# Performance work log

Measured on AMD Instinct MI355X. Metric: run time of the kernel, lower is better.

Reference implementation:

```python
import jax, jax.numpy as jnp
import numpy as np

GRID_H, GRID_W = 128, 128
MODES1, MODES2 = 24, 24
DEPTH = 4
WIDTH = 64
IN_CH = 3
OUT_CH = 1
B, N = 8, 16384
EPS = 1e-5


def _gelu(x):
    return jax.nn.gelu(x, approximate=False)  # torch default (erf) GELU


def setup_inputs() -> dict:
    key = jax.random.key(0)
    ks = jax.random.split(key, 16)
    f32 = jnp.float32

    def lin(k, i, o, std=None):
        s = std if std is not None else 1.0 / np.sqrt(i)
        return (jax.random.normal(k, (i, o), f32) * s).astype(f32)

    scale = 1.0 / (WIDTH * WIDTH)
    sw_shape = (DEPTH, WIDTH, WIDTH, MODES1, MODES2)
    return {
        'coords': jax.random.uniform(ks[0], (B, N, 2), f32, -1.0, 1.0),
        'features': jax.random.normal(ks[1], (B, N, IN_CH), f32),
        'dw0': lin(ks[2], 2, 32), 'db0': jnp.zeros((32,), f32),
        'dw1': lin(ks[3], 32, 32), 'db1': jnp.zeros((32,), f32),
        'dw2': lin(ks[4], 32, 2, std=0.01), 'db2': jnp.zeros((2,), f32),
        'lift_w': lin(ks[5], IN_CH + 2, WIDTH), 'lift_b': jnp.zeros((WIDTH,), f32),
        'sw1r': scale * jax.random.uniform(ks[6], sw_shape, f32),
        'sw1i': scale * jax.random.uniform(ks[7], sw_shape, f32),
        'sw2r': scale * jax.random.uniform(ks[8], sw_shape, f32),
        'sw2i': scale * jax.random.uniform(ks[9], sw_shape, f32),
        'pw_w': (jax.random.normal(ks[10], (DEPTH, WIDTH, WIDTH), f32) / np.sqrt(WIDTH)).astype(f32),
        'pw_b': jnp.zeros((DEPTH, WIDTH), f32),
        'p1_w': lin(ks[11], WIDTH, 128), 'p1_b': jnp.zeros((128,), f32),
        'p2_w': lin(ks[12], 128, OUT_CH), 'p2_b': jnp.zeros((OUT_CH,), f32),
    }


def _spectral_conv2d(x, w1, w2):
    # x: (B, C, H, W); w1/w2: (C_in, C_out, MODES1, MODES2) complex
    Bb, C, H, W = x.shape
    x_ft = jnp.fft.rfft2(x)  # (B, C, H, W//2+1)
    lo = jnp.einsum('bixy,ioxy->boxy', x_ft[:, :, :MODES1, :MODES2], w1)
    hi = jnp.einsum('bixy,ioxy->boxy', x_ft[:, :, -MODES1:, :MODES2], w2)
    out_ft = jnp.zeros((Bb, WIDTH, H, W // 2 + 1), jnp.complex64)
    out_ft = out_ft.at[:, :, :MODES1, :MODES2].set(lo)
    out_ft = out_ft.at[:, :, -MODES1:, :MODES2].set(hi)
    return jnp.fft.irfft2(out_ft, s=(H, W))


def _forward(coords, features, dw0, db0, dw1, db1, dw2, db2, lift_w, lift_b,
             sw1r, sw1i, sw2r, sw2i, pw_w, pw_b, p1_w, p1_b, p2_w, p2_b):
    Bb, Nn, _ = coords.shape
    # 1) deformation: latent = x + MLP(x), clamped to [-1, 1]
    h = _gelu(coords @ dw0 + db0)
    h = _gelu(h @ dw1 + db1)
    latent = jnp.clip(coords + (h @ dw2 + db2), -1.0, 1.0)
    # 2) lifting on concat(features, coords)
    feat = jnp.concatenate([features, coords], axis=-1) @ lift_w + lift_b  # (B,N,width)
    # 3) P2G: nearest-neighbor scatter-mean onto latent grid (align_corners=True)
    ph = (latent[..., 0] + 1.0) * 0.5 * (GRID_H - 1)
    pw = (latent[..., 1] + 1.0) * 0.5 * (GRID_W - 1)
    ih = jnp.clip(jnp.round(ph).astype(jnp.int32), 0, GRID_H - 1)
    iw = jnp.clip(jnp.round(pw).astype(jnp.int32), 0, GRID_W - 1)
    boff = jnp.arange(Bb, dtype=jnp.int32)[:, None] * (GRID_H * GRID_W)
    flat = (boff + ih * GRID_W + iw).reshape(-1)
    nseg = Bb * GRID_H * GRID_W
    sums = jax.ops.segment_sum(feat.reshape(-1, WIDTH), flat, num_segments=nseg)
    cnts = jax.ops.segment_sum(jnp.ones((Bb * Nn, 1), feat.dtype), flat, num_segments=nseg)
    grid = (sums / jnp.maximum(cnts, 1.0)).reshape(Bb, GRID_H, GRID_W, WIDTH)
    grid = grid.transpose(0, 3, 1, 2)  # (B, width, H, W)
    # 4) FNO blocks: gelu(instnorm(spectral(x) + pointwise(x)))
    for d in range(DEPTH):
        w1 = sw1r[d] + 1j * sw1i[d]
        w2 = sw2r[d] + 1j * sw2i[d]
        y = _spectral_conv2d(grid, w1, w2)
        y = y + jnp.einsum('bihw,io->bohw', grid, pw_w[d]) + pw_b[d][None, :, None, None]
        mu = y.mean(axis=(2, 3), keepdims=True)
        var = y.var(axis=(2, 3), keepdims=True)
        grid = _gelu((y - mu) * jax.lax.rsqrt(var + EPS))
    # 5) G2P: bilinear sample latent grid at latent coords
    h0 = jnp.floor(ph)
    w0 = jnp.floor(pw)
    th = (ph - h0)[:, None, :]
    tw = (pw - w0)[:, None, :]
    h0i = jnp.clip(h0.astype(jnp.int32), 0, GRID_H - 1)
    h1i = jnp.clip(h0i + 1, 0, GRID_H - 1)
    w0i = jnp.clip(w0.astype(jnp.int32), 0, GRID_W - 1)
    w1i = jnp.clip(w0i + 1, 0, GRID_W - 1)
    gridf = grid.reshape(Bb, WIDTH, GRID_H * GRID_W)

    def gather(hi_, wi_):
        idx = (hi_ * GRID_W + wi_)[:, None, :]  # (B,1,N)
        return jnp.take_along_axis(gridf, idx, axis=2)  # (B,width,N)

    v00 = gather(h0i, w0i)
    v01 = gather(h0i, w1i)
    v10 = gather(h1i, w0i)
    v11 = gather(h1i, w1i)
    sampled = (v00 * (1 - th) * (1 - tw) + v01 * (1 - th) * tw
               + v10 * th * (1 - tw) + v11 * th * tw)
    sampled = sampled.transpose(0, 2, 1)  # (B,N,width)
    # 6) projection (dropout is identity at eval)
    out = _gelu(sampled @ p1_w + p1_b) @ p2_w + p2_b
    return out  # (B, N, out_channels)


def reference(coords, features, dw0, db0, dw1, db1, dw2, db2, lift_w, lift_b,
              sw1r, sw1i, sw2r, sw2i, pw_w, pw_b, p1_w, p1_b, p2_w, p2_b):
    return _forward(coords, features, dw0, db0, dw1, db1, dw2, db2, lift_w, lift_b,
                    sw1r, sw1i, sw2r, sw2i, pw_w, pw_b, p1_w, p1_b, p2_w, p2_b)
```

## Files before the change

### kernel.cpp

```cpp
#include <hip/hip_runtime.h>
#include <math.h>

#define GH 128
#define GW 128
#define HWC 16384
#define NMODE 1152
#define PI_F 3.14159265358979323846f

typedef _Float16 f16;
typedef __attribute__((ext_vector_type(8))) _Float16 f16x8;
typedef __attribute__((ext_vector_type(4))) float f32x4;

__device__ __forceinline__ float gelu_f(float x) {
  return 0.5f * x * (1.0f + erff(x * 0.70710678118654752f));
}

__device__ __forceinline__ float gelu_fast(float x) {
  float ax = fabsf(x) * 0.70710678118654752f;
  float t = 1.f / fmaf(0.3275911f, ax, 1.f);
  float p = t * fmaf(t, fmaf(t, fmaf(t, fmaf(t, 1.061405429f, -1.453152027f),
                                     1.421413741f), -0.284496736f), 0.254829592f);
  float e = __expf(-ax * ax);
  float r = 1.f - p * e;
  r = copysignf(r, x);
  return 0.5f * x * (1.f + r);
}

__global__ __launch_bounds__(256) void k_twiddle(f16* __restrict__ Fw, f16* __restrict__ Fh,
                                                 f16* __restrict__ Bh, f16* __restrict__ Bw,
                                                 const float* __restrict__ p1w, f16* __restrict__ p1t)
{
  int idx = blockIdx.x * 256 + threadIdx.x;
  if (idx < 6144) {
    int n = idx >> 7, w = idx & 127;
    int ky = n >> 1;
    int ang = (ky * w) & 127;
    float s, c; sincosf((float)ang * (PI_F / 64.f), &s, &c);
    Fw[idx] = (f16)((n & 1) ? -s : c);
  } else if (idx < 18432) {
    int t = idx - 6144;
    int n = t >> 7, h = t & 127;
    int kx = n < 48 ? n : n - 48;
    int f = kx < 24 ? kx : kx + 80;
    int ang = (f * h) & 127;
    float s, c; sincosf((float)ang * (PI_F / 64.f), &s, &c);
    float v = (n < 48) ? c : s;
    Fh[t] = (f16)v;
    Bh[h * 96 + n] = (f16)v;
  } else if (idx < 26624) {
    int t = idx - 18432;
    int w = t >> 6, k = t & 63;
    float v = 0.f;
    if (k < 48 && k != 1) {
      int ky = k >> 1;
      float g = (ky == 0) ? 1.f : 2.f;
      int ang = (ky * w) & 127;
      float s, c; sincosf((float)ang * (PI_F / 64.f), &s, &c);
      v = (k & 1) ? -g * s : g * c;
    }
    Bw[t] = (f16)v;
  } else if (idx < 34816) {
    int t = idx - 26624;
    int j = t >> 6, i = t & 63;
    p1t[t] = (f16)p1w[i * 128 + j];
  }
}

__global__ __launch_bounds__(256) void k_points(
    const float* __restrict__ coords,
    const float* __restrict__ dw0, const float* __restrict__ db0,
    const float* __restrict__ dw1, const float* __restrict__ db1,
    const float* __restrict__ dw2, const float* __restrict__ db2,
    int* __restrict__ cnt_i,
    int* __restrict__ ptrank, int* __restrict__ pd_cell,
    int* __restrict__ pd_idx, float* __restrict__ pd_th, float* __restrict__ pd_tw)
{
  int pid = blockIdx.x * 256 + threadIdx.x;
  float2 c = ((const float2*)coords)[pid];

  float h1[32];
#pragma unroll
  for (int j = 0; j < 32; ++j)
    h1[j] = gelu_f(fmaf(c.x, dw0[j], fmaf(c.y, dw0[32 + j], db0[j])));

  float a[32];
#pragma unroll
  for (int j = 0; j < 32; ++j) a[j] = db1[j];
#pragma unroll 4
  for (int k = 0; k < 32; ++k) {
    float hk = h1[k];
    const float* wr = dw1 + k * 32;
#pragma unroll
    for (int j = 0; j < 32; ++j) a[j] = fmaf(hk, wr[j], a[j]);
  }

  float d0 = db2[0], d1 = db2[1];
#pragma unroll 4
  for (int k = 0; k < 32; ++k) {
    float hk = gelu_f(a[k]);
    d0 = fmaf(hk, dw2[2 * k], d0);
    d1 = fmaf(hk, dw2[2 * k + 1], d1);
  }

  float l0 = fminf(fmaxf(c.x + d0, -1.f), 1.f);
  float l1 = fminf(fmaxf(c.y + d1, -1.f), 1.f);
  float ph = (l0 + 1.f) * 0.5f * 127.f;
  float pw = (l1 + 1.f) * 0.5f * 127.f;
  int ih = min(max((int)rintf(ph), 0), 127);
  int iw = min(max((int)rintf(pw), 0), 127);
  int b = pid >> 14;
  int cell = b * HWC + ih * GW + iw;

  int r = atomicAdd(&cnt_i[cell], 1);
  ptrank[pid] = r;
  pd_cell[pid] = cell;

  float fh = floorf(ph), fw = floorf(pw);
  int h0i = min(max((int)fh, 0), 127), w0i = min(max((int)fw, 0), 127);
  pd_idx[pid] = h0i | (w0i << 8);
  pd_th[pid] = ph - fh;
  pd_tw[pid] = pw - fw;
}

__global__ __launch_bounds__(256) void k_scanA(const int* __restrict__ cnt,
                                               int* __restrict__ starts, int* __restrict__ btot)
{
  __shared__ int sh[256];
  int blk = blockIdx.x, t = threadIdx.x;
  int base = blk * 512;
  int v0 = cnt[base + 2 * t], v1 = cnt[base + 2 * t + 1];
  int pair = v0 + v1;
  sh[t] = pair; __syncthreads();
  int acc = pair;
  for (int off = 1; off < 256; off <<= 1) {
    int add = (t >= off) ? sh[t - off] : 0;
    __syncthreads();
    acc += add; sh[t] = acc;
    __syncthreads();
  }
  int excl = acc - pair;
  starts[base + 2 * t] = excl;
  starts[base + 2 * t + 1] = excl + v0;
  if (t == 255) btot[blk] = acc;
}

__global__ __launch_bounds__(256) void k_scanB(const int* __restrict__ btot, int* __restrict__ boff)
{
  __shared__ int sh[256];
  int t = threadIdx.x;
  int v = btot[t];
  sh[t] = v; __syncthreads();
  int acc = v;
  for (int off = 1; off < 256; off <<= 1) {
    int add = (t >= off) ? sh[t - off] : 0;
    __syncthreads();
    acc += add; sh[t] = acc;
    __syncthreads();
  }
  boff[t] = acc - v;
}

__global__ __launch_bounds__(256) void k_perm(const int* __restrict__ pd_cell, const int* __restrict__ ptrank,
                                              const int* __restrict__ starts, const int* __restrict__ boff,
                                              const int* __restrict__ pd_idx, const float* __restrict__ pd_th,
                                              const float* __restrict__ pd_tw,
                                              const float* __restrict__ coords, const float* __restrict__ feats,
                                              int4* __restrict__ pds,
                                              float4* __restrict__ scA, float* __restrict__ scB)
{
  int pid = blockIdx.x * 256 + threadIdx.x;
  int cell = pd_cell[pid];
  int dst = starts[cell] + boff[cell >> 9] + ptrank[pid];
  int4 rec;
  rec.x = pid;
  rec.y = pd_idx[pid];
  rec.z = __float_as_int(pd_th[pid]);
  rec.w = __float_as_int(pd_tw[pid]);
  pds[dst] = rec;
  float2 c = ((const float2*)coords)[pid];
  scA[dst] = make_float4(feats[pid * 3], feats[pid * 3 + 1], feats[pid * 3 + 2], c.x);
  scB[dst] = c.y;
}

__global__ __launch_bounds__(256) void k_gridlift(const float4* __restrict__ scA, const float* __restrict__ scB,
                                                  const int* __restrict__ starts, const int* __restrict__ boff,
                                                  const int* __restrict__ cnt_i,
                                                  const float* __restrict__ lw,
                                                  const float* __restrict__ lb,
                                                  f16* __restrict__ Gh)
{
  __shared__ float sp[2][128][5];
  __shared__ float s_lw[5][64];
  __shared__ float s_lb[64];
  __shared__ float s_cnt[128];
  int b = blockIdx.y, cbase = blockIdx.x * 128, tid = threadIdx.x;
  int cl = tid & 127, par = tid >> 7;
  int gcell = b * HWC + cbase + cl;
  int start = starts[gcell] + boff[gcell >> 9];
  int cnt = cnt_i[gcell];
  float a0 = 0.f, a1 = 0.f, a2 = 0.f, a3 = 0.f, a4 = 0.f;
  for (int p = start + par; p < start + cnt; p += 2) {
    float4 A = scA[p];
    a0 += A.x; a1 += A.y; a2 += A.z; a3 += A.w; a4 += scB[p];
  }
  sp[par][cl][0] = a0; sp[par][cl][1] = a1; sp[par][cl][2] = a2;
  sp[par][cl][3] = a3; sp[par][cl][4] = a4;
  if (par == 0) s_cnt[cl] = (float)cnt;
  for (int l = tid; l < 320; l += 256) ((float*)s_lw)[l] = lw[l];
  if (tid < 64) s_lb[tid] = lb[tid];
  __syncthreads();
  float v0 = sp[0][cl][0] + sp[1][cl][0];
  float v1 = sp[0][cl][1] + sp[1][cl][1];
  float v2 = sp[0][cl][2] + sp[1][cl][2];
  float v3 = sp[0][cl][3] + sp[1][cl][3];
  float v4 = sp[0][cl][4] + sp[1][cl][4];
  float cntf = s_cnt[cl];
  float inv = 1.f / fmaxf(cntf, 1.f);
  int oh = tid >> 7;
#pragma unroll
  for (int j = 0; j < 32; ++j) {
    int o = oh * 32 + j;
    float val = cntf * s_lb[o];
    val = fmaf(v0, s_lw[0][o], val);
    val = fmaf(v1, s_lw[1][o], val);
    val = fmaf(v2, s_lw[2][o], val);
    val = fmaf(v3, s_lw[3][o], val);
    val = fmaf(v4, s_lw[4][o], val);
    Gh[(size_t)(b * 64 + o) * HWC + cbase + cl] = (f16)(val * inv);
  }
}

__global__ __launch_bounds__(256) void k_fwdpw(const f16* __restrict__ Gh,
                                               const f16* __restrict__ Fw_t, const f16* __restrict__ Fh_t,
                                               float2* __restrict__ Xf2,
                                               const float* __restrict__ pww, const float* __restrict__ pwb,
                                               f16* __restrict__ yh)
{
  __shared__ char smem[52224];
  int tid = threadIdx.x;
  int wave = tid >> 6, lane = tid & 63, lr = lane & 15, lg = lane >> 4;

  if (blockIdx.x < 512) {
    f16 (*s_fw)[136]  = (f16(*)[136])smem;
    f16 (*s_img)[136] = (f16(*)[136])(smem + 13056);
    f16 (*s_xw)[136]  = (f16(*)[136])(smem + 13056);
    f16 (*s_fh)[136]  = (f16(*)[136])(smem + 13056 + 48 * 136 * 2);
    int bc = blockIdx.x;
    for (int l = tid; l < 2048; l += 256) {
      int r = l >> 4, c = l & 15;
      *(f16x8*)&s_img[r][c * 8] = *(const f16x8*)(Gh + (size_t)bc * HWC + r * 128 + c * 8);
    }
    for (int l = tid; l < 768; l += 256) {
      int r = l >> 4, c = l & 15;
      *(f16x8*)&s_fw[r][c * 8] = *(const f16x8*)(Fw_t + r * 128 + c * 8);
    }
    __syncthreads();

    f32x4 acc1[2][3] = {};
#pragma unroll
    for (int ks = 0; ks < 4; ++ks) {
      f16x8 a[2], b[3];
#pragma unroll
      for (int mm = 0; mm < 2; ++mm) a[mm] = *(const f16x8*)&s_img[(wave * 2 + mm) * 16 + lr][ks * 32 + lg * 8];
#pragma unroll
      for (int nt = 0; nt < 3; ++nt) b[nt] = *(const f16x8*)&s_fw[nt * 16 + lr][ks * 32 + lg * 8];
#pragma unroll
      for (int mm = 0; mm < 2; ++mm)
#pragma unroll
        for (int nt = 0; nt < 3; ++nt)
          acc1[mm][nt] = __builtin_amdgcn_mfma_f32_16x16x32_f16(a[mm], b[nt], acc1[mm][nt], 0, 0, 0);
    }
    __syncthreads();
#pragma unroll
    for (int mm = 0; mm < 2; ++mm)
#pragma unroll
      for (int nt = 0; nt < 3; ++nt) {
        int n = nt * 16 + lr;
        int h0 = (wave * 2 + mm) * 16 + lg * 4;
#pragma unroll
        for (int r = 0; r < 4; ++r) s_xw[n][h0 + r] = (f16)acc1[mm][nt][r];
      }
    for (int l = tid; l < 1536; l += 256) {
      int r = l >> 4, c = l & 15;
      *(f16x8*)&s_fh[r][c * 8] = *(const f16x8*)(Fh_t + r * 128 + c * 8);
    }
    __syncthreads();

    for (int u = wave; u < 9; u += 4) {
      int mt = u / 3, ntC = u - mt * 3;
      f32x4 accC = {}, accS = {};
#pragma unroll
      for (int ks = 0; ks < 4; ++ks) {
        f16x8 a  = *(const f16x8*)&s_xw[mt * 16 + lr][ks * 32 + lg * 8];
        f16x8 bC = *(const f16x8*)&s_fh[ntC * 16 + lr][ks * 32 + lg * 8];
        f16x8 bS = *(const f16x8*)&s_fh[(ntC + 3) * 16 + lr][ks * 32 + lg * 8];
        accC = __builtin_amdgcn_mfma_f32_16x16x32_f16(a, bC, accC, 0, 0, 0);
        accS = __builtin_amdgcn_mfma_f32_16x16x32_f16(a, bS, accS, 0, 0, 0);
      }
      int kx = ntC * 16 + lr;
      int ky0 = (mt * 16 + lg * 4) >> 1;
      Xf2[bc * NMODE + kx * 24 + ky0]     = make_float2(accC[0] + accS[1], accC[1] - accS[0]);
      Xf2[bc * NMODE + kx * 24 + ky0 + 1] = make_float2(accC[2] + accS[3], accC[3] - accS[2]);
    }
  } else {
    f16 (*gt)[72] = (f16(*)[72])smem;
    f16 (*wt)[72] = (f16(*)[72])(smem + 36864);
    float* s_b    = (float*)(smem + 46080);
    int blk = blockIdx.x - 512;
    int b = blk >> 6, p0 = (blk & 63) * 256;
    for (int l = tid; l < 4096; l += 256) {
      int i = l >> 6, o = l & 63;
      wt[o][i ^ (((o >> 3) & 7) << 3)] = (f16)pww[l];
    }
    if (tid < 64) s_b[tid] = pwb[tid];
    for (int l = tid; l < 2048; l += 256) {
      int i = l >> 5, pc = (l & 31) * 8;
      f16x8 v = *(const f16x8*)(Gh + (size_t)(b * 64 + i) * HWC + p0 + pc);
      int sw = (l & 7) << 3;
#pragma unroll
      for (int j = 0; j < 8; ++j) gt[pc + j][i ^ sw] = v[j];
    }
    __syncthreads();
    int pw_ = wave * 64;
    f32x4 acc[4][4] = {};
#pragma unroll
    for (int kk = 0; kk < 2; ++kk) {
      f16x8 a[4], bb[4];
#pragma unroll
      for (int mi = 0; mi < 4; ++mi) {
        int o = 16 * mi + lr;
        a[mi] = *(const f16x8*)&wt[o][(kk * 32 + lg * 8) ^ (((o >> 3) & 7) << 3)];
      }
#pragma unroll
      for (int ni = 0; ni < 4; ++ni) {
        int p = pw_ + 16 * ni + lr;
        bb[ni] = *(const f16x8*)&gt[p][(kk * 32 + lg * 8) ^ (((p >> 3) & 7) << 3)];
      }
#pragma unroll
      for (int mi = 0; mi < 4; ++mi)
#pragma unroll
        for (int ni = 0; ni < 4; ++ni)
          acc[mi][ni] = __builtin_amdgcn_mfma_f32_16x16x32_f16(a[mi], bb[ni], acc[mi][ni], 0, 0, 0);
    }
    __syncthreads();
    f16 (*s_o)[264] = (f16(*)[264])smem;
#pragma unroll
    for (int mi = 0; mi < 4; ++mi)
#pragma unroll
      for (int ni = 0; ni < 4; ++ni) {
#pragma unroll
        for (int r = 0; r < 4; ++r) {
          int o = 16 * mi + lg * 4 + r;
          s_o[o][pw_ + 16 * ni + lr] = (f16)(acc[mi][ni][r] + s_b[o]);
        }
      }
    __syncthreads();
    for (int l = tid; l < 2048; l += 256) {
      int o = l >> 5, pc = (l & 31) * 8;
      *(f16x8*)(yh + (size_t)(b * 64 + o) * HWC + p0 + pc) = *(const f16x8*)&s_o[o][pc];
    }
  }
}

__global__ __launch_bounds__(128) void k_mix(const float2* __restrict__ Xf2,
    const float* __restrict__ w1r, const float* __restrict__ w1i,
    const float* __restrict__ w2r, const float* __restrict__ w2i,
    float2* __restrict__ Yp)
{
  int m = blockIdx.x * 64 + (threadIdx.x & 63);
  int o = blockIdx.y * 2 + (threadIdx.x >> 6);
  int half = blockIdx.z >> 2;
  int ic = blockIdx.z & 3;
  int gm = half * 576 + m;
  const float* wr_ = half ? w2r : w1r;
  const float* wi_ = half ? w2i : w1i;
  float aR[8] = {}, aI[8] = {};
  int i0 = ic * 16;
#pragma unroll 4
  for (int ii = 0; ii < 16; ++ii) {
    int i = i0 + ii;
    int widx = (i * 64 + o) * 576 + m;
    float wr = wr_[widx], wi = wi_[widx];
#pragma unroll
    for (int b = 0; b < 8; ++b) {
      float2 x = Xf2[(b * 64 + i) * NMODE + gm];
      aR[b] = fmaf(x.x, wr, aR[b]); aR[b] = fmaf(-x.y, wi, aR[b]);
      aI[b] = fmaf(x.x, wi, aI[b]); aI[b] = fmaf(x.y, wr, aI[b]);
    }
  }
#pragma unroll
  for (int b = 0; b < 8; ++b)
    Yp[(size_t)ic * 589824 + (b * 64 + o) * NMODE + gm] = make_float2(aR[b], aI[b]);
}

__global__ __launch_bounds__(256) void k_inv(const float2* __restrict__ Yp,
                                             const f16* __restrict__ Bh_t, const f16* __restrict__ Bw_t,
                                             const f16* __restrict__ yh, f16* __restrict__ Gh)
{
  __shared__ f16 s_u[21120];
  __shared__ float rs[256], rq[256];
  __shared__ float s_mu, s_rstd;
  f16 (*s_a)[120]  = (f16(*)[120])s_u;
  f16 (*s_bh)[120] = (f16(*)[120])(s_u + 48 * 120);
  f16 (*s_t)[72]   = (f16(*)[72])s_u;
  f16 (*s_bw)[72]  = (f16(*)[72])(s_u + 128 * 72);
  f16 (*s_y)[136]  = (f16(*)[136])s_u;
  int bc = blockIdx.x, tid = threadIdx.x;

  for (int l = tid; l < 1152; l += 256) {
    int kx = l / 24, ky = l - kx * 24;
    float2 y0 = Yp[(size_t)bc * NMODE + l];
    float2 y1 = Yp[589824 + (size_t)bc * NMODE + l];
    float2 y2 = Yp[2 * 589824 + (size_t)bc * NMODE + l];
    float2 y3 = Yp[3 * 589824 + (size_t)bc * NMODE + l];
    float yr = (y0.x + y1.x) + (y2.x + y3.x);
    float yi = (y0.y + y1.y) + (y2.y + y3.y);
    s_a[2 * ky][kx]          = (f16)yr;
    s_a[2 * ky][48 + kx]     = (f16)(-yi);
    s_a[2 * ky + 1][kx]      = (f16)yi;
    s_a[2 * ky + 1][48 + kx] = (f16)yr;
  }
  for (int l = tid; l < 1536; l += 256) {
    int r = l / 12, c = l - r * 12;
    *(f16x8*)&s_bh[r][c * 8] = *(const f16x8*)(Bh_t + r * 96 + c * 8);
  }
  __syncthreads();
  int wave = tid >> 6, lane = tid & 63, lr = lane & 15, lg = lane >> 4;

  f32x4 acc_a[6];
#pragma unroll
  for (int i = 0; i < 6; ++i) acc_a[i] = (f32x4){0.f, 0.f, 0.f, 0.f};
#pragma unroll
  for (int i = 0; i < 6; ++i) {
    int t = wave + 4 * i;
    int mt = t >> 3, nt = t & 7;
#pragma unroll
    for (int ks = 0; ks < 3; ++ks) {
      f16x8 a = *(const f16x8*)&s_a[mt * 16 + lr][ks * 32 + lg * 8];
      f16x8 b = *(const f16x8*)&s_bh[nt * 16 + lr][ks * 32 + lg * 8];
      acc_a[i] = __builtin_amdgcn_mfma_f32_16x16x32_f16(a, b, acc_a[i], 0, 0, 0);
    }
  }
  __syncthreads();
#pragma unroll
  for (int i = 0; i < 6; ++i) {
    int t = wave + 4 * i;
    int mt = t >> 3, nt = t & 7;
    int h = nt * 16 + lr;
    int m0 = mt * 16 + lg * 4;
#pragma unroll
    for (int r = 0; r < 4; ++r) s_t[h][m0 + r] = (f16)acc_a[i][r];
  }
  for (int l = tid; l < 2048; l += 256) {
    int h = l >> 4, c = 48 + (l & 15);
    s_t[h][c] = (f16)0.f;
  }
  for (int l = tid; l < 1024; l += 256) {
    int r = l >> 3, c = l & 7;
    *(f16x8*)&s_bw[r][c * 8] = *(const f16x8*)(Bw_t + r * 64 + c * 8);
  }
  __syncthreads();

  f32x4 acc_b[2][8] = {};
#pragma unroll
  for (int ks = 0; ks < 2; ++ks) {
    f16x8 a[2], b[8];
#pragma unroll
    for (int mm = 0; mm < 2; ++mm) a[mm] = *(const f16x8*)&s_t[(wave * 2 + mm) * 16 + lr][ks * 32 + lg * 8];
#pragma unroll
    for (int nt = 0; nt < 8; ++nt) b[nt] = *(const f16x8*)&s_bw[nt * 16 + lr][ks * 32 + lg * 8];
#pragma unroll
    for (int mm = 0; mm < 2; ++mm)
#pragma unroll
      for (int nt = 0; nt < 8; ++nt)
        acc_b[mm][nt] = __builtin_amdgcn_mfma_f32_16x16x32_f16(a[mm], b[nt], acc_b[mm][nt], 0, 0, 0);
  }
  __syncthreads();
  for (int l = tid; l < 2048; l += 256) {
    int r = l >> 4, c = l & 15;
    *(f16x8*)&s_y[r][c * 8] = *(const f16x8*)(yh + (size_t)bc * HWC + r * 128 + c * 8);
  }
  __syncthreads();
  float sum = 0.f, ssq = 0.f;
#pragma unroll
  for (int mm = 0; mm < 2; ++mm)
#pragma unroll
    for (int nt = 0; nt < 8; ++nt)
#pragma unroll
      for (int r = 0; r < 4; ++r) {
        int h = (wave * 2 + mm) * 16 + lg * 4 + r;
        int w = nt * 16 + lr;
        float v = acc_b[mm][nt][r] * (1.f / 16384.f) + (float)s_y[h][w];
        acc_b[mm][nt][r] = v;
        sum += v; ssq = fmaf(v, v, ssq);
      }
  rs[tid] = sum; rq[tid] = ssq;
  __syncthreads();
  for (int sft = 128; sft > 0; sft >>= 1) {
    if (tid < sft) { rs[tid] += rs[tid + sft]; rq[tid] += rq[tid + sft]; }
    __syncthreads();
  }
  if (tid == 0) {
    float mu = rs[0] * (1.f / 16384.f);
    float var = fmaxf(rq[0] * (1.f / 16384.f) - mu * mu, 0.f);
    s_mu = mu;
    s_rstd = rsqrtf(var + 1e-5f);
  }
  __syncthreads();
  float mu = s_mu, rstd = s_rstd;
#pragma unroll
  for (int mm = 0; mm < 2; ++mm)
#pragma unroll
    for (int nt = 0; nt < 8; ++nt)
#pragma unroll
      for (int r = 0; r < 4; ++r) {
        int h = (wave * 2 + mm) * 16 + lg * 4 + r;
        int w = nt * 16 + lr;
        s_y[h][w] = (f16)gelu_fast((acc_b[mm][nt][r] - mu) * rstd);
      }
  __syncthreads();
  for (int l = tid; l < 2048; l += 256) {
    int r = l >> 4, c = l & 15;
    *(f16x8*)(Gh + (size_t)bc * HWC + r * 128 + c * 8) = *(const f16x8*)&s_y[r][c * 8];
  }
}

__global__ __launch_bounds__(256) void k_tr(const f16* __restrict__ Gh, f16* __restrict__ Gp)
{
  __shared__ f16 t[64][264];
  int b = blockIdx.x >> 6, cell0 = (blockIdx.x & 63) * 256, tid = threadIdx.x;
  for (int l = tid; l < 2048; l += 256) {
    int c = l >> 5, q = l & 31;
    *(f16x8*)&t[c][q * 8] = *(const f16x8*)(Gh + (size_t)(b * 64 + c) * HWC + cell0 + q * 8);
  }
  __syncthreads();
  int cell = tid;
  f16* dst = Gp + ((size_t)b * HWC + cell0 + cell) * 64;
#pragma unroll
  for (int q = 0; q < 8; ++q) {
    f16x8 v;
#pragma unroll
    for (int j = 0; j < 8; ++j) v[j] = t[q * 8 + j][cell];
    *(f16x8*)(dst + q * 8) = v;
  }
}

__global__ __launch_bounds__(256) void k_gather(const f16* __restrict__ Gp,
                                                const int4* __restrict__ pds,
                                                f16* __restrict__ smp)
{
  int idx = blockIdx.x * 256 + threadIdx.x;
  int spt = idx >> 3, c8 = (idx & 7) * 8;
  int4 rec = pds[spt];
  int b = rec.x >> 14;
  int h0 = rec.y & 255, w0 = (rec.y >> 8) & 255;
  int h1 = min(h0 + 1, 127), w1 = min(w0 + 1, 127);
  float th = __int_as_float(rec.z), tw = __int_as_float(rec.w);
  float w00 = (1.f - th) * (1.f - tw), w01 = (1.f - th) * tw;
  float w10 = th * (1.f - tw), w11 = th * tw;
  const f16* base = Gp + (((size_t)b << 14) << 6);
  f16x8 a  = *(const f16x8*)(base + (h0 * 128 + w0) * 64 + c8);
  f16x8 b2 = *(const f16x8*)(base + (h0 * 128 + w1) * 64 + c8);
  f16x8 c  = *(const f16x8*)(base + (h1 * 128 + w0) * 64 + c8);
  f16x8 d  = *(const f16x8*)(base + (h1 * 128 + w1) * 64 + c8);
  f16x8 o;
#pragma unroll
  for (int j = 0; j < 8; ++j)
    o[j] = (f16)(w00 * (float)a[j] + w01 * (float)b2[j] + w10 * (float)c[j] + w11 * (float)d[j]);
  *(f16x8*)(smp + (size_t)spt * 64 + c8) = o;
}

__global__ __launch_bounds__(256) void k_mlp(const f16* __restrict__ smp,
                                             const int4* __restrict__ pds,
                                             const f16* __restrict__ p1t,
                                             const float* __restrict__ p1b,
                                             const float* __restrict__ p2w, const float* __restrict__ p2b,
                                             float* __restrict__ out)
{
  __shared__ f16 s_in[128][72];
  __shared__ f16 s_p1[128][72];
  __shared__ float s_b1[128], s_p2[128];
  int blk = blockIdx.x, tid = threadIdx.x;
  for (int l = tid; l < 1024; l += 256) {
    int row = l >> 3, c8 = (l & 7) * 8;
    *(f16x8*)&s_in[row][c8] = *(const f16x8*)(smp + ((size_t)blk * 128 + row) * 64 + c8);
  }
  for (int l = tid; l < 1024; l += 256) {
    int j = l >> 3, c8 = (l & 7) * 8;
    *(f16x8*)&s_p1[j][c8] = *(const f16x8*)(p1t + j * 64 + c8);
  }
  if (tid < 128) { s_b1[tid] = p1b[tid]; s_p2[tid] = p2w[tid]; }
  __syncthreads();
  int wave = tid >> 6, lane = tid & 63, lr = lane & 15, lg = lane >> 4;
  f32x4 acc[2][8] = {};
#pragma unroll
  for (int ks = 0; ks < 2; ++ks) {
    f16x8 a[2], b[8];
#pragma unroll
    for (int mm = 0; mm < 2; ++mm) a[mm] = *(const f16x8*)&s_in[(wave * 2 + mm) * 16 + lr][ks * 32 + lg * 8];
#pragma unroll
    for (int nt = 0; nt < 8; ++nt) b[nt] = *(const f16x8*)&s_p1[nt * 16 + lr][ks * 32 + lg * 8];
#pragma unroll
    for (int mm = 0; mm < 2; ++mm)
#pragma unroll
      for (int nt = 0; nt < 8; ++nt)
        acc[mm][nt] = __builtin_amdgcn_mfma_f32_16x16x32_f16(a[mm], b[nt], acc[mm][nt], 0, 0, 0);
  }
  float p2b0 = p2b[0];
  float part[2][4] = {};
#pragma unroll
  for (int mm = 0; mm < 2; ++mm)
#pragma unroll
    for (int nt = 0; nt < 8; ++nt) {
#pragma unroll
      for (int r = 0; r < 4; ++r) {
        int j = nt * 16 + lr;
        part[mm][r] += gelu_fast(acc[mm][nt][r] + s_b1[j]) * s_p2[j];
      }
    }
#pragma unroll
  for (int mm = 0; mm < 2; ++mm)
#pragma unroll
    for (int r = 0; r < 4; ++r) {
      float v = part[mm][r];
      v += __shfl_xor(v, 1, 16);
      v += __shfl_xor(v, 2, 16);
      v += __shfl_xor(v, 4, 16);
      v += __shfl_xor(v, 8, 16);
      if (lr == 0) {
        int pt = (wave * 2 + mm) * 16 + lg * 4 + r;
        int opid = pds[blk * 128 + pt].x;
        out[opid] = v + p2b0;
      }
    }
}

extern "C" void kernel_launch(void* const* d_in, const int* in_sizes, int n_in,
                              void* d_out, int out_size, void* d_ws, size_t ws_size,
                              hipStream_t stream) {
  const float* coords = (const float*)d_in[0];
  const float* feats  = (const float*)d_in[1];
  const float* dw0 = (const float*)d_in[2];
  const float* db0 = (const float*)d_in[3];
  const float* dw1 = (const float*)d_in[4];
  const float* db1 = (const float*)d_in[5];
  const float* dw2 = (const float*)d_in[6];
  const float* db2 = (const float*)d_in[7];
  const float* liftw = (const float*)d_in[8];
  const float* liftb = (const float*)d_in[9];
  const float* sw1r = (const float*)d_in[10];
  const float* sw1i = (const float*)d_in[11];
  const float* sw2r = (const float*)d_in[12];
  const float* sw2i = (const float*)d_in[13];
  const float* pww = (const float*)d_in[14];
  const float* pwb = (const float*)d_in[15];
  const float* p1w = (const float*)d_in[16];
  const float* p1b = (const float*)d_in[17];
  const float* p2w = (const float*)d_in[18];
  const float* p2b = (const float*)d_in[19];
  float* out = (float*)d_out;
  char* base = (char*)d_ws;

  int*    cnt_i  = (int*)(base + 0);
  int*    ptrank = (int*)(base + 524288);
  int*    pd_cell= (int*)(base + 1048576);
  int*    starts = (int*)(base + 1572864);
  int*    btot   = (int*)(base + 2097152);
  int*    boff   = (int*)(base + 2098176);
  int*    pd_idx = (int*)(base + 2099200);
  float*  pd_th  = (float*)(base + 2623488);
  float*  pd_tw  = (float*)(base + 3147776);
  f16*    Gh     = (f16*)(base + 8388608);
  f16*    yh     = (f16*)(base + 25165824);
  f16*    smp    = (f16*)(base + 25165824);
  float2* Xf2    = (float2*)(base + 41943040);
  int4*   pds    = (int4*)(base + 51380224);
  f16*    Gp     = (f16*)(base + 53477376);
  float2* Yp     = (float2*)(base + 53477376);
  float4* scA    = (float4*)(base + 70254592);
  float*  scB    = (float*)(base + 72351744);
  f16*    Fw_t   = (f16*)(base + 87031808);
  f16*    Fh_t   = (f16*)(base + 87044096);
  f16*    Bh_t   = (f16*)(base + 87068672);
  f16*    Bw_t   = (f16*)(base + 87093248);
  f16*    p1t    = (f16*)(base + 87109632);

  hipMemsetAsync(cnt_i, 0, 524288, stream);

  k_twiddle<<<136, 256, 0, stream>>>(Fw_t, Fh_t, Bh_t, Bw_t, p1w, p1t);
  k_points<<<512, 256, 0, stream>>>(coords, dw0, db0, dw1, db1, dw2, db2,
                                    cnt_i, ptrank, pd_cell, pd_idx, pd_th, pd_tw);
  k_scanA<<<256, 256, 0, stream>>>(cnt_i, starts, btot);
  k_scanB<<<1, 256, 0, stream>>>(btot, boff);
  k_perm<<<512, 256, 0, stream>>>(pd_cell, ptrank, starts, boff, pd_idx, pd_th, pd_tw,
                                  coords, feats, pds, scA, scB);
  k_gridlift<<<dim3(128, 8), 256, 0, stream>>>(scA, scB, starts, boff, cnt_i, liftw, liftb, Gh);

  for (int d = 0; d < 4; ++d) {
    const int swoff = d * 2359296;
    k_fwdpw<<<1024, 256, 0, stream>>>(Gh, Fw_t, Fh_t, Xf2, pww + d * 4096, pwb + d * 64, yh);
    k_mix<<<dim3(9, 32, 8), 128, 0, stream>>>(Xf2, sw1r + swoff, sw1i + swoff,
                                              sw2r + swoff, sw2i + swoff, Yp);
    k_inv<<<512, 256, 0, stream>>>(Yp, Bh_t, Bw_t, yh, Gh);
  }

  k_tr<<<512, 256, 0, stream>>>(Gh, Gp);
  k_gather<<<4096, 256, 0, stream>>>(Gp, pds, smp);
  k_mlp<<<1024, 256, 0, stream>>>(smp, pds, p1t, p1b, p2w, p2b, out);
}
```

Measured before the change: 324.0 us.

## Vectorize spectral mix loads, store fp16 partials, replace memset with kernel

The spectral mixing kernel now has each thread handle two adjacent modes. It loads them with float4/float2 vector loads, and each block covers four output channels instead of two. The per-chunk partial sums are written as fp16 instead of fp32, which halves the Yp traffic between k_mix and k_inv, and k_inv sums the four partials in fp32. The hipMemsetAsync is replaced by a small zeroing kernel to cut API or launch overhead. Storing the partials in fp16 adds rounding error before the reduction.

```diff
diff --git a/kernel.cpp b/kernel.cpp
--- a/kernel.cpp
+++ b/kernel.cpp
@@ -9,6 +9,8 @@
 
 typedef _Float16 f16;
 typedef __attribute__((ext_vector_type(8))) _Float16 f16x8;
+typedef __attribute__((ext_vector_type(4))) _Float16 f16x4;
+typedef __attribute__((ext_vector_type(2))) _Float16 f16x2;
 typedef __attribute__((ext_vector_type(4))) float f32x4;
 
 __device__ __forceinline__ float gelu_f(float x) {
@@ -24,6 +26,11 @@
   float r = 1.f - p * e;
   r = copysignf(r, x);
   return 0.5f * x * (1.f + r);
+}
+
+__global__ __launch_bounds__(256) void k_zero(int4* __restrict__ p)
+{
+  p[blockIdx.x * 256 + threadIdx.x] = make_int4(0, 0, 0, 0);
 }
 
 __global__ __launch_bounds__(256) void k_twiddle(f16* __restrict__ Fw, f16* __restrict__ Fh,
@@ -365,35 +372,41 @@
 __global__ __launch_bounds__(128) void k_mix(const float2* __restrict__ Xf2,
     const float* __restrict__ w1r, const float* __restrict__ w1i,
     const float* __restrict__ w2r, const float* __restrict__ w2i,
-    float2* __restrict__ Yp)
-{
-  int m = blockIdx.x * 64 + (threadIdx.x & 63);
-  int o = blockIdx.y * 2 + (threadIdx.x >> 6);
+    f16* __restrict__ Yp)
+{
+  int tid = threadIdx.x;
+  int m0 = blockIdx.x * 64 + (tid & 31) * 2;
+  int o  = blockIdx.y * 4 + (tid >> 5);
   int half = blockIdx.z >> 2;
   int ic = blockIdx.z & 3;
-  int gm = half * 576 + m;
+  int gm0 = half * 576 + m0;
   const float* wr_ = half ? w2r : w1r;
   const float* wi_ = half ? w2i : w1i;
-  float aR[8] = {}, aI[8] = {};
+  float aR0[8] = {}, aI0[8] = {}, aR1[8] = {}, aI1[8] = {};
   int i0 = ic * 16;
 #pragma unroll 4
   for (int ii = 0; ii < 16; ++ii) {
     int i = i0 + ii;
-    int widx = (i * 64 + o) * 576 + m;
-    float wr = wr_[widx], wi = wi_[widx];
+    int widx = (i * 64 + o) * 576 + m0;
+    float2 wr2 = *(const float2*)&wr_[widx];
+    float2 wi2 = *(const float2*)&wi_[widx];
 #pragma unroll
     for (int b = 0; b < 8; ++b) {
-      float2 x = Xf2[(b * 64 + i) * NMODE + gm];
-      aR[b] = fmaf(x.x, wr, aR[b]); aR[b] = fmaf(-x.y, wi, aR[b]);
-      aI[b] = fmaf(x.x, wi, aI[b]); aI[b] = fmaf(x.y, wr, aI[b]);
-    }
-  }
-#pragma unroll
-  for (int b = 0; b < 8; ++b)
-    Yp[(size_t)ic * 589824 + (b * 64 + o) * NMODE + gm] = make_float2(aR[b], aI[b]);
-}
-
-__global__ __launch_bounds__(256) void k_inv(const float2* __restrict__ Yp,
+      float4 x = *(const float4*)&Xf2[(b * 64 + i) * NMODE + gm0];
+      aR0[b] = fmaf(x.x, wr2.x, aR0[b]); aR0[b] = fmaf(-x.y, wi2.x, aR0[b]);
+      aI0[b] = fmaf(x.x, wi2.x, aI0[b]); aI0[b] = fmaf(x.y, wr2.x, aI0[b]);
+      aR1[b] = fmaf(x.z, wr2.y, aR1[b]); aR1[b] = fmaf(-x.w, wi2.y, aR1[b]);
+      aI1[b] = fmaf(x.z, wi2.y, aI1[b]); aI1[b] = fmaf(x.w, wr2.y, aI1[b]);
+    }
+  }
+#pragma unroll
+  for (int b = 0; b < 8; ++b) {
+    f16x4 v = { (f16)aR0[b], (f16)aI0[b], (f16)aR1[b], (f16)aI1[b] };
+    *(f16x4*)(Yp + ((size_t)(ic * 512 + b * 64 + o) * NMODE + gm0) * 2) = v;
+  }
+}
+
+__global__ __launch_bounds__(256) void k_inv(const f16* __restrict__ Yp,
                                              const f16* __restrict__ Bh_t, const f16* __restrict__ Bw_t,
                                              const f16* __restrict__ yh, f16* __restrict__ Gh)
 {
@@ -409,12 +422,12 @@
 
   for (int l = tid; l < 1152; l += 256) {
     int kx = l / 24, ky = l - kx * 24;
-    float2 y0 = Yp[(size_t)bc * NMODE + l];
-    float2 y1 = Yp[589824 + (size_t)bc * NMODE + l];
-    float2 y2 = Yp[2 * 589824 + (size_t)bc * NMODE + l];
-    float2 y3 = Yp[3 * 589824 + (size_t)bc * NMODE + l];
-    float yr = (y0.x + y1.x) + (y2.x + y3.x);
-    float yi = (y0.y + y1.y) + (y2.y + y3.y);
+    float yr = 0.f, yi = 0.f;
+#pragma unroll
+    for (int ic = 0; ic < 4; ++ic) {
+      f16x2 v = *(const f16x2*)(Yp + ((size_t)(ic * 512 + bc) * NMODE + l) * 2);
+      yr += (float)v[0]; yi += (float)v[1];
+    }
     s_a[2 * ky][kx]          = (f16)yr;
     s_a[2 * ky][48 + kx]     = (f16)(-yi);
     s_a[2 * ky + 1][kx]      = (f16)yi;
@@ -676,7 +689,7 @@
   float2* Xf2    = (float2*)(base + 41943040);
   int4*   pds    = (int4*)(base + 51380224);
   f16*    Gp     = (f16*)(base + 53477376);
-  float2* Yp     = (float2*)(base + 53477376);
+  f16*    Yp     = (f16*)(base + 53477376);
   float4* scA    = (float4*)(base + 70254592);
   float*  scB    = (float*)(base + 72351744);
   f16*    Fw_t   = (f16*)(base + 87031808);
@@ -685,8 +698,7 @@
   f16*    Bw_t   = (f16*)(base + 87093248);
   f16*    p1t    = (f16*)(base + 87109632);
 
-  hipMemsetAsync(cnt_i, 0, 524288, stream);
-
+  k_zero<<<128, 256, 0, stream>>>((int4*)cnt_i);
   k_twiddle<<<136, 256, 0, stream>>>(Fw_t, Fh_t, Bh_t, Bw_t, p1w, p1t);
   k_points<<<512, 256, 0, stream>>>(coords, dw0, db0, dw1, db1, dw2, db2,
                                     cnt_i, ptrank, pd_cell, pd_idx, pd_th, pd_tw);
@@ -699,7 +711,7 @@
   for (int d = 0; d < 4; ++d) {
     const int swoff = d * 2359296;
     k_fwdpw<<<1024, 256, 0, stream>>>(Gh, Fw_t, Fh_t, Xf2, pww + d * 4096, pwb + d * 64, yh);
-    k_mix<<<dim3(9, 32, 8), 128, 0, stream>>>(Xf2, sw1r + swoff, sw1i + swoff,
+    k_mix<<<dim3(9, 16, 8), 128, 0, stream>>>(Xf2, sw1r + swoff, sw1i + swoff,
                                               sw2r + swoff, sw2i + swoff, Yp);
     k_inv<<<512, 256, 0, stream>>>(Yp, Bh_t, Bw_t, yh, Gh);
   }
```

Result: slower. 337.3 us (+4.1%).

## Store forward spectrum in fp16 and stage it through shared memory in mix kernel

Applied to the files above, without the earlier changes.

The forward-FFT output modes are written as half-precision complex pairs instead of float2, which halves the intermediate buffer traffic. The mixing kernel now loads its 8x16x64 tile of spectral inputs cooperatively into LDS with vector loads and reads them from there, instead of each thread issuing scattered global loads. The counter memset is replaced with a small zeroing kernel. Reduced precision of the spectral coefficients may cost some accuracy.

```diff
diff --git a/kernel.cpp b/kernel.cpp
--- a/kernel.cpp
+++ b/kernel.cpp
@@ -9,6 +9,7 @@
 
 typedef _Float16 f16;
 typedef __attribute__((ext_vector_type(8))) _Float16 f16x8;
+typedef __attribute__((ext_vector_type(2))) _Float16 f16x2;
 typedef __attribute__((ext_vector_type(4))) float f32x4;
 
 __device__ __forceinline__ float gelu_f(float x) {
@@ -24,6 +25,11 @@
   float r = 1.f - p * e;
   r = copysignf(r, x);
   return 0.5f * x * (1.f + r);
+}
+
+__global__ __launch_bounds__(256) void k_zero(int4* __restrict__ p)
+{
+  p[blockIdx.x * 256 + threadIdx.x] = make_int4(0, 0, 0, 0);
 }
 
 __global__ __launch_bounds__(256) void k_twiddle(f16* __restrict__ Fw, f16* __restrict__ Fh,
@@ -232,7 +238,7 @@
 
 __global__ __launch_bounds__(256) void k_fwdpw(const f16* __restrict__ Gh,
                                                const f16* __restrict__ Fw_t, const f16* __restrict__ Fh_t,
-                                               float2* __restrict__ Xf2,
+                                               f16x2* __restrict__ Xh,
                                                const float* __restrict__ pww, const float* __restrict__ pwb,
                                                f16* __restrict__ yh)
 {
@@ -299,8 +305,10 @@
       }
       int kx = ntC * 16 + lr;
       int ky0 = (mt * 16 + lg * 4) >> 1;
-      Xf2[bc * NMODE + kx * 24 + ky0]     = make_float2(accC[0] + accS[1], accC[1] - accS[0]);
-      Xf2[bc * NMODE + kx * 24 + ky0 + 1] = make_float2(accC[2] + accS[3], accC[3] - accS[2]);
+      f16x2 v0 = { (f16)(accC[0] + accS[1]), (f16)(accC[1] - accS[0]) };
+      f16x2 v1 = { (f16)(accC[2] + accS[3]), (f16)(accC[3] - accS[2]) };
+      Xh[bc * NMODE + kx * 24 + ky0]     = v0;
+      Xh[bc * NMODE + kx * 24 + ky0 + 1] = v1;
     }
   } else {
     f16 (*gt)[72] = (f16(*)[72])smem;
@@ -362,32 +370,42 @@
   }
 }
 
-__global__ __launch_bounds__(128) void k_mix(const float2* __restrict__ Xf2,
+__global__ __launch_bounds__(128) void k_mix(const f16x2* __restrict__ Xh,
     const float* __restrict__ w1r, const float* __restrict__ w1i,
     const float* __restrict__ w2r, const float* __restrict__ w2i,
     float2* __restrict__ Yp)
 {
-  int m = blockIdx.x * 64 + (threadIdx.x & 63);
-  int o = blockIdx.y * 2 + (threadIdx.x >> 6);
+  __shared__ f16x2 sx[8][16][64];
+  int tid = threadIdx.x;
   int half = blockIdx.z >> 2;
   int ic = blockIdx.z & 3;
-  int gm = half * 576 + m;
+  int i0 = ic * 16;
+  int mbase = half * 576 + blockIdx.x * 64;
+  for (int l = tid; l < 2048; l += 128) {
+    int row = l >> 4, c4 = (l & 15) * 4;
+    int b = row >> 4, ii = row & 15;
+    *(int4*)&sx[b][ii][c4] = *(const int4*)(Xh + (b * 64 + i0 + ii) * NMODE + mbase + c4);
+  }
+  __syncthreads();
+  int mloc = blockIdx.x * 64 + (tid & 63);
+  int o = blockIdx.y * 2 + (tid >> 6);
   const float* wr_ = half ? w2r : w1r;
   const float* wi_ = half ? w2i : w1i;
   float aR[8] = {}, aI[8] = {};
-  int i0 = ic * 16;
-#pragma unroll 4
+  int m = tid & 63;
+#pragma unroll
   for (int ii = 0; ii < 16; ++ii) {
-    int i = i0 + ii;
-    int widx = (i * 64 + o) * 576 + m;
+    int widx = ((i0 + ii) * 64 + o) * 576 + mloc;
     float wr = wr_[widx], wi = wi_[widx];
 #pragma unroll
     for (int b = 0; b < 8; ++b) {
-      float2 x = Xf2[(b * 64 + i) * NMODE + gm];
-      aR[b] = fmaf(x.x, wr, aR[b]); aR[b] = fmaf(-x.y, wi, aR[b]);
-      aI[b] = fmaf(x.x, wi, aI[b]); aI[b] = fmaf(x.y, wr, aI[b]);
-    }
-  }
+      f16x2 xv = sx[b][ii][m];
+      float xr = (float)xv[0], xi = (float)xv[1];
+      aR[b] = fmaf(xr, wr, aR[b]); aR[b] = fmaf(-xi, wi, aR[b]);
+      aI[b] = fmaf(xr, wi, aI[b]); aI[b] = fmaf(xi, wr, aI[b]);
+    }
+  }
+  int gm = half * 576 + mloc;
 #pragma unroll
   for (int b = 0; b < 8; ++b)
     Yp[(size_t)ic * 589824 + (b * 64 + o) * NMODE + gm] = make_float2(aR[b], aI[b]);
@@ -673,7 +691,7 @@
   f16*    Gh     = (f16*)(base + 8388608);
   f16*    yh     = (f16*)(base + 25165824);
   f16*    smp    = (f16*)(base + 25165824);
-  float2* Xf2    = (float2*)(base + 41943040);
+  f16x2*  Xh     = (f16x2*)(base + 41943040);
   int4*   pds    = (int4*)(base + 51380224);
   f16*    Gp     = (f16*)(base + 53477376);
   float2* Yp     = (float2*)(base + 53477376);
@@ -685,8 +703,7 @@
   f16*    Bw_t   = (f16*)(base + 87093248);
   f16*    p1t    = (f16*)(base + 87109632);
 
-  hipMemsetAsync(cnt_i, 0, 524288, stream);
-
+  k_zero<<<128, 256, 0, stream>>>((int4*)cnt_i);
   k_twiddle<<<136, 256, 0, stream>>>(Fw_t, Fh_t, Bh_t, Bw_t, p1w, p1t);
   k_points<<<512, 256, 0, stream>>>(coords, dw0, db0, dw1, db1, dw2, db2,
                                     cnt_i, ptrank, pd_cell, pd_idx, pd_th, pd_tw);
@@ -698,8 +715,8 @@
 
   for (int d = 0; d < 4; ++d) {
     const int swoff = d * 2359296;
-    k_fwdpw<<<1024, 256, 0, stream>>>(Gh, Fw_t, Fh_t, Xf2, pww + d * 4096, pwb + d * 64, yh);
-    k_mix<<<dim3(9, 32, 8), 128, 0, stream>>>(Xf2, sw1r + swoff, sw1i + swoff,
+    k_fwdpw<<<1024, 256, 0, stream>>>(Gh, Fw_t, Fh_t, Xh, pww + d * 4096, pwb + d * 64, yh);
+    k_mix<<<dim3(9, 32, 8), 128, 0, stream>>>(Xh, sw1r + swoff, sw1i + swoff,
                                               sw2r + swoff, sw2i + swoff, Yp);
     k_inv<<<512, 256, 0, stream>>>(Yp, Bh_t, Bw_t, yh, Gh);
   }
```

Measured after the change: 346.9 us. 7.0% more time.
